# Kernel tuning notes

Measured on AMD Instinct MI355X. Metric: run time of the kernel, lower is better.

## Reference

```python
import jax, jax.numpy as jnp
import numpy as np

B, S, N, H = 16, 512, 64, 768
E_TYPES, R_TYPES = 9, 10


def setup_inputs() -> dict:
    key = jax.random.key(0)
    ks = jax.random.split(key, 8)
    seq = jax.random.normal(ks[0], (B, S, H), dtype=jnp.float32)
    starts = jax.random.randint(ks[1], (B, N), 0, S - 16)
    lengths = jax.random.randint(ks[2], (B, N), 1, 16)
    entity_spans = jnp.stack([starts, starts + lengths], axis=-1).astype(jnp.int32)  # [B,N,2], start<end<=S
    attention_mask = jnp.ones((B, S), dtype=jnp.int32)
    sc = 0.02
    return {
        "sequence_output": seq,
        "attention_mask": attention_mask,
        "entity_spans": entity_spans,
        "W1e": jax.random.normal(ks[3], (H, H // 2), dtype=jnp.float32) * sc,
        "b1e": jnp.zeros((H // 2,), dtype=jnp.float32),
        "W2e": jax.random.normal(ks[4], (H // 2, E_TYPES), dtype=jnp.float32) * sc,
        "b2e": jnp.zeros((E_TYPES,), dtype=jnp.float32),
        "W1r": jax.random.normal(ks[5], (2 * H, H), dtype=jnp.float32) * sc,
        "b1r": jnp.zeros((H,), dtype=jnp.float32),
        "W2r": jax.random.normal(ks[6], (H, R_TYPES), dtype=jnp.float32) * sc,
        "b2r": jnp.zeros((R_TYPES,), dtype=jnp.float32),
    }


def reference(sequence_output, attention_mask, entity_spans,
              W1e, b1e, W2e, b2e, W1r, b1r, W2r, b2r):
    # Entity classifier over all tokens (dropout = identity in eval mode).
    # entity_logits: [B, S, E_TYPES]
    entity_logits = jax.nn.relu(sequence_output @ W1e + b1e) @ W2e + b2e

    # Span-mean entity representations, vectorized (replaces the Python
    # per-entity loop with .item() syncs). span mask: [B, N, S]
    pos = jnp.arange(S, dtype=entity_spans.dtype)
    start = entity_spans[..., 0:1]
    end = entity_spans[..., 1:2]
    span_mask = ((pos >= start) & (pos < end)).astype(sequence_output.dtype)
    counts = jnp.maximum(span_mask.sum(-1, keepdims=True), 1.0)
    # entity_repr: [B, N, H] = mean over tokens in each span
    entity_repr = jnp.einsum('bns,bsh->bnh', span_mask, sequence_output) / counts

    # Relation classification for all ordered pairs i<j (replaces nested
    # per-pair micro-launches with one batched GEMM).
    ii, jj = jnp.triu_indices(N, k=1)  # static, P = N*(N-1)/2
    pair_repr = jnp.concatenate([entity_repr[:, ii, :], entity_repr[:, jj, :]], axis=-1)  # [B,P,2H]
    relation_logits = jax.nn.relu(pair_repr @ W1r + b1r) @ W2r + b2r  # [B,P,R_TYPES]

    return entity_logits, entity_repr, relation_logits
```

## Files before the change

### kernel.cpp

```cpp
#include <hip/hip_runtime.h>
#include <hip/hip_bf16.h>


#define S_LEN 512
#define H_DIM 768
#define NPAIR 2016

typedef __bf16 bf16x8 __attribute__((ext_vector_type(8)));
typedef float f32x4 __attribute__((ext_vector_type(4)));

__device__ __forceinline__ void gload_lds16(const void* g, void* l) {
    __builtin_amdgcn_global_load_lds(
        (const __attribute__((address_space(1))) void*)g,
        (__attribute__((address_space(3))) void*)l, 16, 0, 0);
}

__device__ __forceinline__ ushort f2bf(float x) {
    __hip_bfloat16 h = __float2bfloat16(x);
    return *(ushort*)&h;
}

__device__ __forceinline__ void bf8_to_f32(const ushort* p, float* f) {
    const uint* u = (const uint*)p;
    #pragma unroll
    for (int i = 0; i < 4; ++i) {
        uint x = u[i];
        f[2 * i]     = __uint_as_float(x << 16);
        f[2 * i + 1] = __uint_as_float(x & 0xffff0000u);
    }
}

__global__ __launch_bounds__(256) void prep_all_k(
    const float* __restrict__ seq, const int* __restrict__ spans,
    const float* __restrict__ W1e, const float* __restrict__ W1r,
    const float* __restrict__ W2e, const float* __restrict__ W2r,
    const float* __restrict__ b1r,
    float* __restrict__ erep, ushort* __restrict__ erep_bf,
    ushort* __restrict__ W1et, ushort* __restrict__ W1rt,
    ushort* __restrict__ W2et, ushort* __restrict__ W2rt,
    float* __restrict__ b1r_ext, ushort* __restrict__ seq_bf)
{
    __shared__ float t[32][33];
    const int bid = blockIdx.x, tid = threadIdx.x;

    if (bid < 1024) {
        const int bn = bid, b = bn >> 6;
        const int s0 = spans[bn * 2], s1 = spans[bn * 2 + 1];
        int lo = s0 < 0 ? 0 : s0;
        int hi = s1 > S_LEN ? S_LEN : s1;
        int cnt = hi - lo;
        if (cnt < 1) cnt = 1;
        const float inv = 1.f / (float)cnt;
        for (int c = tid; c < H_DIM; c += 256) {
            float acc = 0.f;
            for (int s = lo; s < hi; ++s)
                acc += seq[((size_t)b * S_LEN + s) * H_DIM + c];
            float v = acc * inv;
            erep[(size_t)bn * H_DIM + c] = v;
            erep_bf[(size_t)bn * H_DIM + c] = f2bf(v);
        }
    } else if (bid < 2464) {
        const float* src; ushort* dst; int b2, C;
        if (bid < 1312)      { b2 = bid - 1024; src = W1e; dst = W1et; C = 384; }
        else if (bid < 1888) { b2 = bid - 1312; src = W1r; dst = W1rt; C = 768; }
        else                 { b2 = bid - 1888; src = W1r + 768 * 768; dst = W1rt + 768 * 768; C = 768; }
        const int br = b2 % 24, bc = b2 / 24;
        const int r = tid >> 5, c = tid & 31;
        #pragma unroll
        for (int p = 0; p < 4; ++p) {
            int rr = r + p * 8;
            t[rr][c] = src[(size_t)(br * 32 + rr) * C + bc * 32 + c];
        }
        __syncthreads();
        #pragma unroll
        for (int p = 0; p < 4; ++p) {
            int rr = r + p * 8;
            dst[(size_t)(bc * 32 + rr) * 768 + br * 32 + c] = f2bf(t[c][rr]);
        }
    } else if (bid < 2542) {
        int idx = (bid - 2464) * 256 + tid;
        if (idx < 12288) {
            int col = idx / 768, k = idx % 768;
            W2rt[idx] = (col < 10) ? f2bf(W2r[k * 10 + col]) : (ushort)0;
        } else if (idx < 18432) {
            int u = idx - 12288;
            int col = u / 384, k = u % 384;
            W2et[u] = (col < 9) ? f2bf(W2e[k * 9 + col]) : (ushort)0;
        } else {
            int u = idx - 18432;
            b1r_ext[u] = (u < 768) ? b1r[u] : 0.f;
        }
    } else {
        for (int i = (bid - 2542) * 256 + tid; i < (8192 * 768) / 4; i += 1024 * 256) {
            float4 v = ((const float4*)seq)[i];
            ushort4 o;
            o.x = f2bf(v.x); o.y = f2bf(v.y); o.z = f2bf(v.z); o.w = f2bf(v.w);
            ((ushort4*)seq_bf)[i] = o;
        }
    }
}

template<int EPI>
__device__ __forceinline__ void gemm_body(
    const ushort* __restrict__ A, const ushort* __restrict__ Bt,
    const float* __restrict__ bias, void* __restrict__ Cout,
    int bx, int by, int N, int K, ushort* As, ushort* Bs)
{
    const int tid = threadIdx.x;
    const int lane = tid & 63, wid = tid >> 6;
    const int wr = wid >> 1, wc = wid & 1;
    const int m0 = by * 64, n0 = bx * 128;
    const int fr = lane & 15, kg = lane >> 4;

    const int srow = tid >> 2, skq = (tid & 3) * 8;
    const ushort* ag0 = A + (size_t)(m0 + srow) * K + skq;
    const ushort* bg0 = Bt + (size_t)(n0 + srow) * K + skq;
    const ushort* bg1 = Bt + (size_t)(n0 + 64 + srow) * K + skq;

    int aoff[2], boff[4];
    #pragma unroll
    for (int i = 0; i < 2; ++i)
        aoff[i] = (wr * 32 + i * 16 + fr) * 32 + kg * 8;
    #pragma unroll
    for (int i = 0; i < 4; ++i)
        boff[i] = (wc * 64 + i * 16 + fr) * 32 + kg * 8;

    const int nsteps = K / 32;

    auto STAGE = [&](int kt, int buf) {
        const int kn = kt * 32;
        gload_lds16(ag0 + kn, As + buf * 2048 + tid * 8);
        gload_lds16(bg0 + kn, Bs + buf * 4096 + tid * 8);
        gload_lds16(bg1 + kn, Bs + buf * 4096 + 2048 + tid * 8);
    };

    STAGE(0, 0);
    STAGE(1, 1);
    STAGE(2, 2);

    f32x4 acc[2][4] = {};

    for (int t = 0; t < nsteps; ++t) {
        if (t < nsteps - 2)       asm volatile("s_waitcnt vmcnt(6)" ::: "memory");
        else if (t == nsteps - 2) asm volatile("s_waitcnt vmcnt(3)" ::: "memory");
        else                      asm volatile("s_waitcnt vmcnt(0)" ::: "memory");
        __builtin_amdgcn_s_barrier();
        __builtin_amdgcn_sched_barrier(0);
        if (t + 3 < nsteps) STAGE(t + 3, (t + 3) & 3);
        const int buf = t & 3;
        bf16x8 af[2], bv[4];
        #pragma unroll
        for (int i = 0; i < 2; ++i) af[i] = *(const bf16x8*)&As[buf * 2048 + aoff[i]];
        #pragma unroll
        for (int i = 0; i < 4; ++i) bv[i] = *(const bf16x8*)&Bs[buf * 4096 + boff[i]];
        #pragma unroll
        for (int mi = 0; mi < 2; ++mi)
            #pragma unroll
            for (int nj = 0; nj < 4; ++nj)
                acc[mi][nj] = __builtin_amdgcn_mfma_f32_16x16x32_bf16(
                    af[mi], bv[nj], acc[mi][nj], 0, 0, 0);
    }

    __hip_bfloat16* Cb = (__hip_bfloat16*)Cout;
    float bcol[4];
    #pragma unroll
    for (int nj = 0; nj < 4; ++nj) bcol[nj] = bias[n0 + wc * 64 + nj * 16 + fr];
    #pragma unroll
    for (int mi = 0; mi < 2; ++mi)
        #pragma unroll
        for (int j = 0; j < 4; ++j) {
            size_t rb = (size_t)(m0 + wr * 32 + mi * 16 + kg * 4 + j) * N
                      + n0 + wc * 64 + fr;
            #pragma unroll
            for (int nj = 0; nj < 4; ++nj) {
                float v = acc[mi][nj][j] + bcol[nj];
                if (EPI == 0) v = fmaxf(v, 0.f);
                Cb[rb + nj * 16] = __float2bfloat16(v);
            }
        }
}

__global__ __launch_bounds__(256) void gemm2_k(
    const ushort* __restrict__ seq_bf, const ushort* __restrict__ W1et,
    const float* __restrict__ b1e, ushort* __restrict__ H1bf,
    const ushort* __restrict__ erep_bf, const ushort* __restrict__ W1rt,
    const float* __restrict__ b1r_ext, ushort* __restrict__ UVbf)
{
    __shared__ ushort As[4 * 2048];
    __shared__ ushort Bs[4 * 4096];
    const int bid = blockIdx.x;
    if (bid < 384) {
        gemm_body<0>(seq_bf, W1et, b1e, H1bf, bid % 3, bid / 3, 384, 768, As, Bs);
    } else {
        const int b2 = bid - 384;
        gemm_body<2>(erep_bf, W1rt, b1r_ext, UVbf, b2 % 12, b2 / 12, 1536, 768, As, Bs);
    }
}

__global__ __launch_bounds__(256) void post_k(
    const ushort* __restrict__ UVbf, const ushort* __restrict__ W2rt,
    const float* __restrict__ b2r, float* __restrict__ rlog,
    const ushort* __restrict__ H1, const ushort* __restrict__ W2et,
    const float* __restrict__ b2e, float* __restrict__ elog)
{
    const int tid = threadIdx.x;
    const int lane = tid & 63, wid = tid >> 6;
    const int fr = lane & 15, kg = lane >> 4;
    const int bid = blockIdx.x;

    if (bid < 160) {
        const int t = bid % 10, b = bid / 10;
        int it, jt;
        if (t < 4)      { it = 0; jt = t; }
        else if (t < 7) { it = 1; jt = t - 3; }
        else if (t < 9) { it = 2; jt = t - 5; }
        else            { it = 3; jt = 3; }
        const int i0 = it * 16, j0 = jt * 16;
        const ushort* Ub = UVbf + (size_t)(b * 64 + i0) * 1536;
        const ushort* Vb = UVbf + (size_t)(b * 64 + j0) * 1536 + 768;

        f32x4 acc[4] = {};

        for (int c = 0; c < 24; ++c) {
            const int kk = c * 32 + kg * 8;
            const bf16x8 bv = *(const bf16x8*)(W2rt + fr * 768 + kk);
            float fv[8];
            bf8_to_f32(Vb + (size_t)fr * 1536 + kk, fv);
            #pragma unroll
            for (int q = 0; q < 4; ++q) {
                float fu[8];
                bf8_to_f32(Ub + (size_t)(wid * 4 + q) * 1536 + kk, fu);
                ushort h[8];
                #pragma unroll
                for (int e = 0; e < 8; ++e)
                    h[e] = f2bf(fmaxf(fu[e] + fv[e], 0.f));
                bf16x8 av = *(bf16x8*)h;
                acc[q] = __builtin_amdgcn_mfma_f32_16x16x32_bf16(av, bv, acc[q], 0, 0, 0);
            }
        }

        if (fr < 10) {
            const float bias = b2r[fr];
            #pragma unroll
            for (int q = 0; q < 4; ++q) {
                const int i = i0 + wid * 4 + q;
                #pragma unroll
                for (int jr = 0; jr < 4; ++jr) {
                    const int j = j0 + kg * 4 + jr;
                    if (j > i) {
                        int p = i * 63 - i * (i - 1) / 2 + (j - i - 1);
                        rlog[((size_t)(b * NPAIR + p)) * 10 + fr] = acc[q][jr] + bias;
                    }
                }
            }
        }
    } else {
        const int rbase = (bid - 160) * 64 + wid * 16;
        f32x4 acc = {};
        #pragma unroll
        for (int c = 0; c < 12; ++c) {
            const int kk = c * 32 + kg * 8;
            bf16x8 av = *(const bf16x8*)(H1 + (size_t)(rbase + fr) * 384 + kk);
            bf16x8 bv = *(const bf16x8*)(W2et + fr * 384 + kk);
            acc = __builtin_amdgcn_mfma_f32_16x16x32_bf16(av, bv, acc, 0, 0, 0);
        }
        if (fr < 9) {
            const float bias = b2e[fr];
            #pragma unroll
            for (int j = 0; j < 4; ++j)
                elog[(size_t)(rbase + kg * 4 + j) * 9 + fr] = acc[j] + bias;
        }
    }
}

extern "C" void kernel_launch(void* const* d_in, const int* in_sizes, int n_in,
                              void* d_out, int out_size, void* d_ws, size_t ws_size,
                              hipStream_t stream)
{
    const float* seq   = (const float*)d_in[0];
    const int*   spans = (const int*)d_in[2];
    const float* W1e   = (const float*)d_in[3];
    const float* b1e   = (const float*)d_in[4];
    const float* W2e   = (const float*)d_in[5];
    const float* b2e   = (const float*)d_in[6];
    const float* W1r   = (const float*)d_in[7];
    const float* b1r   = (const float*)d_in[8];
    const float* W2r   = (const float*)d_in[9];
    const float* b2r   = (const float*)d_in[10];

    float* out  = (float*)d_out;
    float* elog = out;
    float* erep = out + 73728;
    float* rlog = out + 73728 + 786432;

    char* ws = (char*)d_ws;
    ushort* seq_bf  = (ushort*)ws;
    ushort* W1et    = (ushort*)(ws + 12582912);
    ushort* W1rt    = (ushort*)(ws + 13172736);
    ushort* erep_bf = (ushort*)(ws + 15532032);
    ushort* H1bf    = (ushort*)(ws + 17104896);
    ushort* W2rt    = (ushort*)(ws + 23396352);
    ushort* W2et    = (ushort*)(ws + 23420928);
    float*  b1r_ext = (float*) (ws + 23433216);
    ushort* UVbf    = (ushort*)(ws + 23439360);

    prep_all_k<<<3566, 256, 0, stream>>>(seq, spans, W1e, W1r, W2e, W2r, b1r,
                                         erep, erep_bf, W1et, W1rt, W2et, W2rt,
                                         b1r_ext, seq_bf);
    gemm2_k<<<576, 256, 0, stream>>>(seq_bf, W1et, b1e, H1bf,
                                     erep_bf, W1rt, b1r_ext, UVbf);
    post_k<<<288, 256, 0, stream>>>(UVbf, W2rt, b2r, rlog,
                                    H1bf, W2et, b2e, elog);
}
```

Before: 141.3 us.

## Fuse fp32-to-bf16 sequence conversion into GEMM A-tile loads with swizzled LDS

Removes the separate pass that converts the whole fp32 sequence to bf16 in the prep kernel. The entity GEMM now streams fp32 A tiles straight into LDS and converts them to bf16 in registers before the MFMA. LDS layouts for A and B get an XOR swizzle to avoid bank conflicts, and the waitcnt depths are adjusted for the extra loads. This saves a 25MB read/write round trip but doubles A-tile LDS traffic and footprint (64KB shared per block), which may reduce occupancy.

Result: slower. 153.4 us (+8.5%).

```diff
diff --git a/kernel.cpp b/kernel.cpp
--- a/kernel.cpp
+++ b/kernel.cpp
@@ -38,7 +38,7 @@
     float* __restrict__ erep, ushort* __restrict__ erep_bf,
     ushort* __restrict__ W1et, ushort* __restrict__ W1rt,
     ushort* __restrict__ W2et, ushort* __restrict__ W2rt,
-    float* __restrict__ b1r_ext, ushort* __restrict__ seq_bf)
+    float* __restrict__ b1r_ext)
 {
     __shared__ float t[32][33];
     const int bid = blockIdx.x, tid = threadIdx.x;
@@ -77,7 +77,7 @@
             int rr = r + p * 8;
             dst[(size_t)(bc * 32 + rr) * 768 + br * 32 + c] = f2bf(t[c][rr]);
         }
-    } else if (bid < 2542) {
+    } else {
         int idx = (bid - 2464) * 256 + tid;
         if (idx < 12288) {
             int col = idx / 768, k = idx % 768;
@@ -86,25 +86,18 @@
             int u = idx - 12288;
             int col = u / 384, k = u % 384;
             W2et[u] = (col < 9) ? f2bf(W2e[k * 9 + col]) : (ushort)0;
-        } else {
+        } else if (idx < 19968) {
             int u = idx - 18432;
             b1r_ext[u] = (u < 768) ? b1r[u] : 0.f;
         }
-    } else {
-        for (int i = (bid - 2542) * 256 + tid; i < (8192 * 768) / 4; i += 1024 * 256) {
-            float4 v = ((const float4*)seq)[i];
-            ushort4 o;
-            o.x = f2bf(v.x); o.y = f2bf(v.y); o.z = f2bf(v.z); o.w = f2bf(v.w);
-            ((ushort4*)seq_bf)[i] = o;
-        }
-    }
-}
-
-template<int EPI>
+    }
+}
+
+template<int EPI, bool AF32>
 __device__ __forceinline__ void gemm_body(
-    const ushort* __restrict__ A, const ushort* __restrict__ Bt,
+    const void* __restrict__ Ap, const ushort* __restrict__ Bt,
     const float* __restrict__ bias, void* __restrict__ Cout,
-    int bx, int by, int N, int K, ushort* As, ushort* Bs)
+    int bx, int by, int N, int K, char* As, char* Bs)
 {
     const int tid = threadIdx.x;
     const int lane = tid & 63, wid = tid >> 6;
@@ -112,26 +105,51 @@
     const int m0 = by * 64, n0 = bx * 128;
     const int fr = lane & 15, kg = lane >> 4;
 
-    const int srow = tid >> 2, skq = (tid & 3) * 8;
-    const ushort* ag0 = A + (size_t)(m0 + srow) * K + skq;
-    const ushort* bg0 = Bt + (size_t)(n0 + srow) * K + skq;
-    const ushort* bg1 = Bt + (size_t)(n0 + 64 + srow) * K + skq;
-
-    int aoff[2], boff[4];
-    #pragma unroll
-    for (int i = 0; i < 2; ++i)
-        aoff[i] = (wr * 32 + i * 16 + fr) * 32 + kg * 8;
-    #pragma unroll
-    for (int i = 0; i < 4; ++i)
-        boff[i] = (wc * 64 + i * 16 + fr) * 32 + kg * 8;
+    constexpr int ABUF = AF32 ? 8192 : 4096;
+
+    const int sB_row = tid >> 2;
+    const int sB_q   = (tid & 3) ^ ((sB_row >> 1) & 3);
+    const ushort* bg0 = Bt + (size_t)(n0 + sB_row) * K + sB_q * 8;
+    const ushort* bg1 = bg0 + (size_t)64 * K;
+    const ushort* ag16 = nullptr;
+    const float *agA = nullptr, *agB = nullptr;
+    if constexpr (AF32) {
+        const int r = tid >> 3, q = (tid & 7) ^ ((tid >> 3) & 7);
+        agA = (const float*)Ap + (size_t)(m0 + r) * K + q * 4;
+        agB = agA + (size_t)32 * K;
+    } else {
+        ag16 = (const ushort*)Ap + (size_t)(m0 + sB_row) * K + sB_q * 8;
+    }
+
+    int aoff0[2], aoff1[2], boffs[4];
+    #pragma unroll
+    for (int i = 0; i < 2; ++i) {
+        const int row = wr * 32 + i * 16 + fr;
+        if constexpr (AF32) {
+            aoff0[i] = row * 128 + (((2 * kg)     ^ (row & 7)) * 16);
+            aoff1[i] = row * 128 + (((2 * kg + 1) ^ (row & 7)) * 16);
+        } else {
+            aoff0[i] = row * 64 + ((kg ^ ((row >> 1) & 3)) * 16);
+        }
+    }
+    #pragma unroll
+    for (int i = 0; i < 4; ++i) {
+        const int col = wc * 64 + i * 16 + fr;
+        boffs[i] = col * 64 + ((kg ^ ((col >> 1) & 3)) * 16);
+    }
 
     const int nsteps = K / 32;
 
     auto STAGE = [&](int kt, int buf) {
         const int kn = kt * 32;
-        gload_lds16(ag0 + kn, As + buf * 2048 + tid * 8);
-        gload_lds16(bg0 + kn, Bs + buf * 4096 + tid * 8);
-        gload_lds16(bg1 + kn, Bs + buf * 4096 + 2048 + tid * 8);
+        if constexpr (AF32) {
+            gload_lds16(agA + kn, As + buf * ABUF + tid * 16);
+            gload_lds16(agB + kn, As + buf * ABUF + 4096 + tid * 16);
+        } else {
+            gload_lds16(ag16 + kn, As + buf * ABUF + tid * 16);
+        }
+        gload_lds16(bg0 + kn, Bs + buf * 8192 + tid * 16);
+        gload_lds16(bg1 + kn, Bs + buf * 8192 + 4096 + tid * 16);
     };
 
     STAGE(0, 0);
@@ -141,18 +159,36 @@
     f32x4 acc[2][4] = {};
 
     for (int t = 0; t < nsteps; ++t) {
-        if (t < nsteps - 2)       asm volatile("s_waitcnt vmcnt(6)" ::: "memory");
-        else if (t == nsteps - 2) asm volatile("s_waitcnt vmcnt(3)" ::: "memory");
-        else                      asm volatile("s_waitcnt vmcnt(0)" ::: "memory");
+        if (t < nsteps - 2) {
+            if constexpr (AF32) asm volatile("s_waitcnt vmcnt(8)" ::: "memory");
+            else                asm volatile("s_waitcnt vmcnt(6)" ::: "memory");
+        } else if (t == nsteps - 2) {
+            if constexpr (AF32) asm volatile("s_waitcnt vmcnt(4)" ::: "memory");
+            else                asm volatile("s_waitcnt vmcnt(3)" ::: "memory");
+        } else {
+            asm volatile("s_waitcnt vmcnt(0)" ::: "memory");
+        }
         __builtin_amdgcn_s_barrier();
         __builtin_amdgcn_sched_barrier(0);
         if (t + 3 < nsteps) STAGE(t + 3, (t + 3) & 3);
         const int buf = t & 3;
         bf16x8 af[2], bv[4];
         #pragma unroll
-        for (int i = 0; i < 2; ++i) af[i] = *(const bf16x8*)&As[buf * 2048 + aoff[i]];
-        #pragma unroll
-        for (int i = 0; i < 4; ++i) bv[i] = *(const bf16x8*)&Bs[buf * 4096 + boff[i]];
+        for (int i = 0; i < 2; ++i) {
+            if constexpr (AF32) {
+                f32x4 x0 = *(const f32x4*)(As + buf * ABUF + aoff0[i]);
+                f32x4 x1 = *(const f32x4*)(As + buf * ABUF + aoff1[i]);
+                ushort h[8] __attribute__((aligned(16))) =
+                    { f2bf(x0[0]), f2bf(x0[1]), f2bf(x0[2]), f2bf(x0[3]),
+                      f2bf(x1[0]), f2bf(x1[1]), f2bf(x1[2]), f2bf(x1[3]) };
+                af[i] = *(bf16x8*)h;
+            } else {
+                af[i] = *(const bf16x8*)(As + buf * ABUF + aoff0[i]);
+            }
+        }
+        #pragma unroll
+        for (int i = 0; i < 4; ++i)
+            bv[i] = *(const bf16x8*)(Bs + buf * 8192 + boffs[i]);
         #pragma unroll
         for (int mi = 0; mi < 2; ++mi)
             #pragma unroll
@@ -181,19 +217,19 @@
 }
 
 __global__ __launch_bounds__(256) void gemm2_k(
-    const ushort* __restrict__ seq_bf, const ushort* __restrict__ W1et,
+    const float* __restrict__ seq, const ushort* __restrict__ W1et,
     const float* __restrict__ b1e, ushort* __restrict__ H1bf,
     const ushort* __restrict__ erep_bf, const ushort* __restrict__ W1rt,
     const float* __restrict__ b1r_ext, ushort* __restrict__ UVbf)
 {
-    __shared__ ushort As[4 * 2048];
-    __shared__ ushort Bs[4 * 4096];
+    __shared__ char As[4 * 8192];
+    __shared__ char Bs[4 * 8192];
     const int bid = blockIdx.x;
     if (bid < 384) {
-        gemm_body<0>(seq_bf, W1et, b1e, H1bf, bid % 3, bid / 3, 384, 768, As, Bs);
+        gemm_body<0, true>(seq, W1et, b1e, H1bf, bid % 3, bid / 3, 384, 768, As, Bs);
     } else {
         const int b2 = bid - 384;
-        gemm_body<2>(erep_bf, W1rt, b1r_ext, UVbf, b2 % 12, b2 / 12, 1536, 768, As, Bs);
+        gemm_body<2, false>(erep_bf, W1rt, b1r_ext, UVbf, b2 % 12, b2 / 12, 1536, 768, As, Bs);
     }
 }
 
@@ -230,7 +266,7 @@
             for (int q = 0; q < 4; ++q) {
                 float fu[8];
                 bf8_to_f32(Ub + (size_t)(wid * 4 + q) * 1536 + kk, fu);
-                ushort h[8];
+                ushort h[8] __attribute__((aligned(16)));
                 #pragma unroll
                 for (int e = 0; e < 8; ++e)
                     h[e] = f2bf(fmaxf(fu[e] + fv[e], 0.f));
@@ -294,20 +330,19 @@
     float* rlog = out + 73728 + 786432;
 
     char* ws = (char*)d_ws;
-    ushort* seq_bf  = (ushort*)ws;
-    ushort* W1et    = (ushort*)(ws + 12582912);
-    ushort* W1rt    = (ushort*)(ws + 13172736);
-    ushort* erep_bf = (ushort*)(ws + 15532032);
-    ushort* H1bf    = (ushort*)(ws + 17104896);
-    ushort* W2rt    = (ushort*)(ws + 23396352);
-    ushort* W2et    = (ushort*)(ws + 23420928);
-    float*  b1r_ext = (float*) (ws + 23433216);
-    ushort* UVbf    = (ushort*)(ws + 23439360);
-
-    prep_all_k<<<3566, 256, 0, stream>>>(seq, spans, W1e, W1r, W2e, W2r, b1r,
+    ushort* W1et    = (ushort*)(ws + 0);
+    ushort* W1rt    = (ushort*)(ws + 589824);
+    ushort* erep_bf = (ushort*)(ws + 2949120);
+    ushort* H1bf    = (ushort*)(ws + 4521984);
+    ushort* W2rt    = (ushort*)(ws + 10813440);
+    ushort* W2et    = (ushort*)(ws + 10838016);
+    float*  b1r_ext = (float*) (ws + 10850304);
+    ushort* UVbf    = (ushort*)(ws + 10856448);
+
+    prep_all_k<<<2542, 256, 0, stream>>>(seq, spans, W1e, W1r, W2e, W2r, b1r,
                                          erep, erep_bf, W1et, W1rt, W2et, W2rt,
-                                         b1r_ext, seq_bf);
-    gemm2_k<<<576, 256, 0, stream>>>(seq_bf, W1et, b1e, H1bf,
+                                         b1r_ext);
+    gemm2_k<<<576, 256, 0, stream>>>(seq, W1et, b1e, H1bf,
                                      erep_bf, W1rt, b1r_ext, UVbf);
     post_k<<<288, 256, 0, stream>>>(UVbf, W2rt, b2r, rlog,
                                     H1bf, W2et, b2e, elog);
```
